# Optimization experiments

Measured on AMD Instinct MI355X. Metric: run time of the kernel, lower is better.

The kernel has to match this reference:

```python
import jax, jax.numpy as jnp
import numpy as np

B, L, M, F = 64, 1024, 256, 256


def setup_inputs() -> dict:
    key = jax.random.key(0)
    k1, k2 = jax.random.split(key)
    patch_features = jax.random.normal(k1, (B, L, F), dtype=jnp.float32)
    queue = jax.random.normal(k2, (L, M, F), dtype=jnp.float32)
    return {"patch_features": patch_features, "queue": queue}


def reference(patch_features, queue):
    # sim[b, l, m] = <patch_features[b, l], queue[l, m]>  (batched per-location matmul)
    sim = jnp.einsum('blf,lmf->blm', patch_features, queue)
    # original takes topk(5) then keeps only index 0 == argmax over memory slots
    idx = jnp.argmax(sim, axis=-1)                      # [B, L]
    # N[b, l] = queue[l, idx[b, l]]
    N = queue[jnp.arange(queue.shape[0])[None, :], idx]  # [B, L, F]
    return N
```

## Files before the change

kernel.cpp:

```cpp
#include <hip/hip_runtime.h>

#define B_ 64
#define L_ 1024
#define M_ 256
#define F_ 256

typedef __attribute__((ext_vector_type(8))) short short8;
typedef __attribute__((ext_vector_type(16))) float f32x16;
typedef unsigned int u32;

struct Frag3 { short8 h, m, l; };

__device__ __forceinline__ u32 asu(float f) { union { float f; u32 u; } c; c.f = f; return c.u; }
__device__ __forceinline__ float asf(u32 u) { union { float f; u32 u; } c; c.u = u; return c.f; }
__device__ __forceinline__ u32 pack2(u32 lo, u32 hi) {
    return __builtin_amdgcn_perm(hi, lo, 0x07060302u);
}
__device__ __forceinline__ float4 ld4(const float* p) {
    return *reinterpret_cast<const float4*>(p);
}

__device__ __forceinline__ void async_cp16(const float* g, float* l) {
    __builtin_amdgcn_global_load_lds(
        (const __attribute__((address_space(1))) u32*)g,
        (__attribute__((address_space(3))) u32*)l,
        16, 0, 0);
}

__device__ __forceinline__ Frag3 split8(float4 a, float4 b) {
    float x[8] = {a.x, a.y, a.z, a.w, b.x, b.y, b.z, b.w};
    u32 xb[8], rb[8], sb[8];
#pragma unroll
    for (int e = 0; e < 8; ++e) {
        xb[e] = asu(x[e]);
        float hf = asf(xb[e] & 0xFFFF0000u);
        float r  = x[e] - hf;
        rb[e] = asu(r);
        float mf = asf(rb[e] & 0xFFFF0000u);
        float r2 = r - mf;
        sb[e] = asu(r2);
    }
    union { u32 w[4]; short8 s; } H, M, Lo;
#pragma unroll
    for (int d = 0; d < 4; ++d) {
        H.w[d]  = pack2(xb[2 * d], xb[2 * d + 1]);
        M.w[d]  = pack2(rb[2 * d], rb[2 * d + 1]);
        Lo.w[d] = pack2(sb[2 * d], sb[2 * d + 1]);
    }
    Frag3 f; f.h = H.s; f.m = M.s; f.l = Lo.s; return f;
}

#define MFMA6(ACC, A, Bf)                                                        \
    ACC = __builtin_amdgcn_mfma_f32_32x32x16_bf16((A).m, (Bf).m, ACC, 0, 0, 0);  \
    ACC = __builtin_amdgcn_mfma_f32_32x32x16_bf16((A).h, (Bf).l, ACC, 0, 0, 0);  \
    ACC = __builtin_amdgcn_mfma_f32_32x32x16_bf16((A).l, (Bf).h, ACC, 0, 0, 0);  \
    ACC = __builtin_amdgcn_mfma_f32_32x32x16_bf16((A).h, (Bf).m, ACC, 0, 0, 0);  \
    ACC = __builtin_amdgcn_mfma_f32_32x32x16_bf16((A).m, (Bf).h, ACC, 0, 0, 0);  \
    ACC = __builtin_amdgcn_mfma_f32_32x32x16_bf16((A).h, (Bf).h, ACC, 0, 0, 0)

__launch_bounds__(256, 2)
__global__ void mq_mfma_lds_kernel(const float* __restrict__ patch,
                                   const float* __restrict__ queue,
                                   float* __restrict__ out) {
    const int l    = blockIdx.x;
    const int t    = threadIdx.x;
    const int lane = t & 63;
    const int w    = t >> 6;
    const int bt   = w & 1;
    const int mtg  = w >> 1;
    const int r32  = lane & 31;
    const int kh   = lane >> 5;

    __shared__ __align__(16) float Ql[2][256 * 32];
    __shared__ __align__(16) float Pl[2][64 * 32];

    const int lrow = lane >> 3;
    const int lcol = lane & 7;
    const float* qsrcw = queue + ((size_t)l * M_ + w * 64 + lrow) * F_ + (lcol ^ lrow) * 4;
    const float* psrcw = patch + ((size_t)(w * 16 + lrow) * L_ + l) * F_ + (lcol ^ lrow) * 4;

#define STAGE(FT, BUF)                                                            \
    {                                                                             \
        _Pragma("unroll")                                                         \
        for (int k = 0; k < 8; ++k)                                               \
            async_cp16(qsrcw + (size_t)k * 8 * F_ + (FT) * 32,                    \
                       &Ql[BUF][(w * 8 + k) * 256]);                              \
        _Pragma("unroll")                                                         \
        for (int k = 0; k < 2; ++k)                                               \
            async_cp16(psrcw + (size_t)k * 8 * L_ * F_ + (FT) * 32,               \
                       &Pl[BUF][(w * 2 + k) * 256]);                              \
    }

    f32x16 acc[4];
#pragma unroll
    for (int mt = 0; mt < 4; ++mt) acc[mt] = (f32x16)0.f;

    STAGE(0, 0);

    const int s7 = r32 & 7;
    const int ra = bt * 32 + r32;

#pragma unroll 1
    for (int ft = 0; ft < 8; ++ft) {
        __builtin_amdgcn_s_barrier();
        __builtin_amdgcn_sched_barrier(0);
        if (ft < 7) {
            STAGE(ft + 1, (ft + 1) & 1);
            asm volatile("s_waitcnt vmcnt(10)" ::: "memory");
        } else {
            asm volatile("s_waitcnt vmcnt(0)" ::: "memory");
        }
        __builtin_amdgcn_sched_barrier(0);
        __builtin_amdgcn_s_barrier();
        __builtin_amdgcn_sched_barrier(0);

        const float* Qb = Ql[ft & 1];
        const float* Pb = Pl[ft & 1];
#pragma unroll
        for (int kk = 0; kk < 2; ++kk) {
            const int c0 = kk * 4 + kh * 2;
            const float4 a0 = ld4(&Pb[ra * 32 + ((c0 ^ s7) * 4)]);
            const float4 a1 = ld4(&Pb[ra * 32 + (((c0 + 1) ^ s7) * 4)]);
            const Frag3 A = split8(a0, a1);
#pragma unroll
            for (int mt = 0; mt < 4; ++mt) {
                const int rb = mtg * 128 + mt * 32 + r32;
                const float4 b0 = ld4(&Qb[rb * 32 + ((c0 ^ s7) * 4)]);
                const float4 b1 = ld4(&Qb[rb * 32 + (((c0 + 1) ^ s7) * 4)]);
                const Frag3 Bf = split8(b0, b1);
                MFMA6(acc[mt], A, Bf);
            }
        }
    }

    __syncthreads();

    float* pval = (float*)&Pl[0][0];
    int*   pidx = (int*)&Pl[0][0] + 128;
    int*   sidx = (int*)&Pl[0][0] + 256;
#pragma unroll
    for (int r = 0; r < 16; ++r) {
        float bv = acc[0][r];
        int   bi = mtg * 128 + r32;
#pragma unroll
        for (int mt = 1; mt < 4; ++mt) {
            const float cv = acc[mt][r];
            const int   ci = mtg * 128 + mt * 32 + r32;
            if (cv > bv) { bv = cv; bi = ci; }
        }
#pragma unroll
        for (int off = 16; off >= 1; off >>= 1) {
            const float ov = __shfl_xor(bv, off);
            const int   oi = __shfl_xor(bi, off);
            if (ov > bv || (ov == bv && oi < bi)) { bv = ov; bi = oi; }
        }
        if (r32 == 0) {
            const int b = bt * 32 + (r & 3) + 8 * (r >> 2) + 4 * kh;
            pval[mtg * 64 + b] = bv;
            pidx[mtg * 64 + b] = bi;
        }
    }
    __syncthreads();

    if (t < 64) {
        const float v0 = pval[t], v1 = pval[64 + t];
        sidx[t] = (v1 > v0) ? pidx[64 + t] : pidx[t];
    }
    __syncthreads();

    const int cb = t >> 6;
    const int cc = t & 63;
#pragma unroll
    for (int b0 = 0; b0 < 64; b0 += 4) {
        const int b  = b0 + cb;
        const int mi = sidx[b];
        const float4 v = ld4(&queue[((size_t)l * M_ + mi) * F_ + cc * 4]);
        *reinterpret_cast<float4*>(&out[((size_t)b * L_ + l) * F_ + cc * 4]) = v;
    }
}

extern "C" void kernel_launch(void* const* d_in, const int* in_sizes, int n_in,
                              void* d_out, int out_size, void* d_ws, size_t ws_size,
                              hipStream_t stream) {
    const float* patch = (const float*)d_in[0];
    const float* queue = (const float*)d_in[1];
    float* out = (float*)d_out;
    mq_mfma_lds_kernel<<<dim3(L_), dim3(256), 0, stream>>>(patch, queue, out);
}
```

Before: 105.9 us.

## Use 512 threads per block, splitting memory slots across eight waves

```diff
diff --git a/kernel.cpp b/kernel.cpp
--- a/kernel.cpp
+++ b/kernel.cpp
@@ -58,7 +58,7 @@
     ACC = __builtin_amdgcn_mfma_f32_32x32x16_bf16((A).m, (Bf).h, ACC, 0, 0, 0);  \
     ACC = __builtin_amdgcn_mfma_f32_32x32x16_bf16((A).h, (Bf).h, ACC, 0, 0, 0)
 
-__launch_bounds__(256, 2)
+__launch_bounds__(512, 2)
 __global__ void mq_mfma_lds_kernel(const float* __restrict__ patch,
                                    const float* __restrict__ queue,
                                    float* __restrict__ out) {
@@ -76,29 +76,26 @@
 
     const int lrow = lane >> 3;
     const int lcol = lane & 7;
-    const float* qsrcw = queue + ((size_t)l * M_ + w * 64 + lrow) * F_ + (lcol ^ lrow) * 4;
-    const float* psrcw = patch + ((size_t)(w * 16 + lrow) * L_ + l) * F_ + (lcol ^ lrow) * 4;
+    const float* qsrcw = queue + ((size_t)l * M_ + w * 32 + lrow) * F_ + (lcol ^ lrow) * 4;
+    const float* psrcw = patch + ((size_t)(w * 8 + lrow) * L_ + l) * F_ + (lcol ^ lrow) * 4;
 
 #define STAGE(FT, BUF)                                                            \
     {                                                                             \
         _Pragma("unroll")                                                         \
-        for (int k = 0; k < 8; ++k)                                               \
+        for (int k = 0; k < 4; ++k)                                               \
             async_cp16(qsrcw + (size_t)k * 8 * F_ + (FT) * 32,                    \
-                       &Ql[BUF][(w * 8 + k) * 256]);                              \
-        _Pragma("unroll")                                                         \
-        for (int k = 0; k < 2; ++k)                                               \
-            async_cp16(psrcw + (size_t)k * 8 * L_ * F_ + (FT) * 32,               \
-                       &Pl[BUF][(w * 2 + k) * 256]);                              \
+                       &Ql[BUF][(w * 4 + k) * 256]);                              \
+        async_cp16(psrcw + (FT) * 32, &Pl[BUF][w * 256]);                         \
     }
 
-    f32x16 acc[4];
-#pragma unroll
-    for (int mt = 0; mt < 4; ++mt) acc[mt] = (f32x16)0.f;
+    f32x16 acc0 = (f32x16)0.f, acc1 = (f32x16)0.f;
 
     STAGE(0, 0);
 
     const int s7 = r32 & 7;
     const int ra = bt * 32 + r32;
+    const int rb0 = mtg * 64 + r32;
+    const int rb1 = mtg * 64 + 32 + r32;
 
 #pragma unroll 1
     for (int ft = 0; ft < 8; ++ft) {
@@ -106,7 +103,7 @@
         __builtin_amdgcn_sched_barrier(0);
         if (ft < 7) {
             STAGE(ft + 1, (ft + 1) & 1);
-            asm volatile("s_waitcnt vmcnt(10)" ::: "memory");
+            asm volatile("s_waitcnt vmcnt(5)" ::: "memory");
         } else {
             asm volatile("s_waitcnt vmcnt(0)" ::: "memory");
         }
@@ -122,13 +119,17 @@
             const float4 a0 = ld4(&Pb[ra * 32 + ((c0 ^ s7) * 4)]);
             const float4 a1 = ld4(&Pb[ra * 32 + (((c0 + 1) ^ s7) * 4)]);
             const Frag3 A = split8(a0, a1);
-#pragma unroll
-            for (int mt = 0; mt < 4; ++mt) {
-                const int rb = mtg * 128 + mt * 32 + r32;
-                const float4 b0 = ld4(&Qb[rb * 32 + ((c0 ^ s7) * 4)]);
-                const float4 b1 = ld4(&Qb[rb * 32 + (((c0 + 1) ^ s7) * 4)]);
+            {
+                const float4 b0 = ld4(&Qb[rb0 * 32 + ((c0 ^ s7) * 4)]);
+                const float4 b1 = ld4(&Qb[rb0 * 32 + (((c0 + 1) ^ s7) * 4)]);
                 const Frag3 Bf = split8(b0, b1);
-                MFMA6(acc[mt], A, Bf);
+                MFMA6(acc0, A, Bf);
+            }
+            {
+                const float4 b0 = ld4(&Qb[rb1 * 32 + ((c0 ^ s7) * 4)]);
+                const float4 b1 = ld4(&Qb[rb1 * 32 + (((c0 + 1) ^ s7) * 4)]);
+                const Frag3 Bf = split8(b0, b1);
+                MFMA6(acc1, A, Bf);
             }
         }
     }
@@ -136,16 +137,15 @@
     __syncthreads();
 
     float* pval = (float*)&Pl[0][0];
-    int*   pidx = (int*)&Pl[0][0] + 128;
-    int*   sidx = (int*)&Pl[0][0] + 256;
+    int*   pidx = (int*)&Pl[0][0] + 256;
+    int*   sidx = (int*)&Pl[0][0] + 512;
 #pragma unroll
     for (int r = 0; r < 16; ++r) {
-        float bv = acc[0][r];
-        int   bi = mtg * 128 + r32;
-#pragma unroll
-        for (int mt = 1; mt < 4; ++mt) {
-            const float cv = acc[mt][r];
-            const int   ci = mtg * 128 + mt * 32 + r32;
+        float bv = acc0[r];
+        int   bi = mtg * 64 + r32;
+        {
+            const float cv = acc1[r];
+            const int   ci = mtg * 64 + 32 + r32;
             if (cv > bv) { bv = cv; bi = ci; }
         }
 #pragma unroll
@@ -163,15 +163,21 @@
     __syncthreads();
 
     if (t < 64) {
-        const float v0 = pval[t], v1 = pval[64 + t];
-        sidx[t] = (v1 > v0) ? pidx[64 + t] : pidx[t];
+        float bv = pval[t];
+        int   bi = pidx[t];
+#pragma unroll
+        for (int g = 1; g < 4; ++g) {
+            const float cv = pval[g * 64 + t];
+            if (cv > bv) { bv = cv; bi = pidx[g * 64 + t]; }
+        }
+        sidx[t] = bi;
     }
     __syncthreads();
 
     const int cb = t >> 6;
     const int cc = t & 63;
 #pragma unroll
-    for (int b0 = 0; b0 < 64; b0 += 4) {
+    for (int b0 = 0; b0 < 64; b0 += 8) {
         const int b  = b0 + cb;
         const int mi = sidx[b];
         const float4 v = ld4(&queue[((size_t)l * M_ + mi) * F_ + cc * 4]);
@@ -185,5 +191,5 @@
     const float* patch = (const float*)d_in[0];
     const float* queue = (const float*)d_in[1];
     float* out = (float*)d_out;
-    mq_mfma_lds_kernel<<<dim3(L_), dim3(256), 0, stream>>>(patch, queue, out);
+    mq_mfma_lds_kernel<<<dim3(L_), dim3(512), 0, stream>>>(patch, queue, out);
 }
```

New measurement: 103.5 us. 2.3% less time.

## Drop LDS double buffering to single buffer for higher block occupancy

Applied to the files above, without the earlier changes.

```diff
diff --git a/kernel.cpp b/kernel.cpp
--- a/kernel.cpp
+++ b/kernel.cpp
@@ -59,7 +59,7 @@
     ACC = __builtin_amdgcn_mfma_f32_32x32x16_bf16((A).h, (Bf).h, ACC, 0, 0, 0)
 
 __launch_bounds__(256, 2)
-__global__ void mq_mfma_lds_kernel(const float* __restrict__ patch,
+__global__ void mq_mfma_sb4_kernel(const float* __restrict__ patch,
                                    const float* __restrict__ queue,
                                    float* __restrict__ out) {
     const int l    = blockIdx.x;
@@ -71,31 +71,17 @@
     const int r32  = lane & 31;
     const int kh   = lane >> 5;
 
-    __shared__ __align__(16) float Ql[2][256 * 32];
-    __shared__ __align__(16) float Pl[2][64 * 32];
+    __shared__ __align__(16) float Ql[256 * 32];
+    __shared__ __align__(16) float Pl[64 * 32];
 
     const int lrow = lane >> 3;
     const int lcol = lane & 7;
     const float* qsrcw = queue + ((size_t)l * M_ + w * 64 + lrow) * F_ + (lcol ^ lrow) * 4;
     const float* psrcw = patch + ((size_t)(w * 16 + lrow) * L_ + l) * F_ + (lcol ^ lrow) * 4;
 
-#define STAGE(FT, BUF)                                                            \
-    {                                                                             \
-        _Pragma("unroll")                                                         \
-        for (int k = 0; k < 8; ++k)                                               \
-            async_cp16(qsrcw + (size_t)k * 8 * F_ + (FT) * 32,                    \
-                       &Ql[BUF][(w * 8 + k) * 256]);                              \
-        _Pragma("unroll")                                                         \
-        for (int k = 0; k < 2; ++k)                                               \
-            async_cp16(psrcw + (size_t)k * 8 * L_ * F_ + (FT) * 32,               \
-                       &Pl[BUF][(w * 2 + k) * 256]);                              \
-    }
-
     f32x16 acc[4];
 #pragma unroll
     for (int mt = 0; mt < 4; ++mt) acc[mt] = (f32x16)0.f;
-
-    STAGE(0, 0);
 
     const int s7 = r32 & 7;
     const int ra = bt * 32 + r32;
@@ -104,29 +90,31 @@
     for (int ft = 0; ft < 8; ++ft) {
         __builtin_amdgcn_s_barrier();
         __builtin_amdgcn_sched_barrier(0);
-        if (ft < 7) {
-            STAGE(ft + 1, (ft + 1) & 1);
-            asm volatile("s_waitcnt vmcnt(10)" ::: "memory");
-        } else {
-            asm volatile("s_waitcnt vmcnt(0)" ::: "memory");
+        {
+            const int o = ft * 32;
+#pragma unroll
+            for (int k = 0; k < 8; ++k)
+                async_cp16(qsrcw + (size_t)k * 8 * F_ + o, &Ql[(w * 8 + k) * 256]);
+#pragma unroll
+            for (int k = 0; k < 2; ++k)
+                async_cp16(psrcw + (size_t)k * 8 * L_ * F_ + o, &Pl[(w * 2 + k) * 256]);
         }
+        asm volatile("s_waitcnt vmcnt(0)" ::: "memory");
         __builtin_amdgcn_sched_barrier(0);
         __builtin_amdgcn_s_barrier();
         __builtin_amdgcn_sched_barrier(0);
 
-        const float* Qb = Ql[ft & 1];
-        const float* Pb = Pl[ft & 1];
 #pragma unroll
         for (int kk = 0; kk < 2; ++kk) {
             const int c0 = kk * 4 + kh * 2;
-            const float4 a0 = ld4(&Pb[ra * 32 + ((c0 ^ s7) * 4)]);
-            const float4 a1 = ld4(&Pb[ra * 32 + (((c0 + 1) ^ s7) * 4)]);
+            const float4 a0 = ld4(&Pl[ra * 32 + ((c0 ^ s7) * 4)]);
+            const float4 a1 = ld4(&Pl[ra * 32 + (((c0 + 1) ^ s7) * 4)]);
             const Frag3 A = split8(a0, a1);
 #pragma unroll
             for (int mt = 0; mt < 4; ++mt) {
                 const int rb = mtg * 128 + mt * 32 + r32;
-                const float4 b0 = ld4(&Qb[rb * 32 + ((c0 ^ s7) * 4)]);
-                const float4 b1 = ld4(&Qb[rb * 32 + (((c0 + 1) ^ s7) * 4)]);
+                const float4 b0 = ld4(&Ql[rb * 32 + ((c0 ^ s7) * 4)]);
+                const float4 b1 = ld4(&Ql[rb * 32 + (((c0 + 1) ^ s7) * 4)]);
                 const Frag3 Bf = split8(b0, b1);
                 MFMA6(acc[mt], A, Bf);
             }
@@ -135,9 +123,9 @@
 
     __syncthreads();
 
-    float* pval = (float*)&Pl[0][0];
-    int*   pidx = (int*)&Pl[0][0] + 128;
-    int*   sidx = (int*)&Pl[0][0] + 256;
+    float* pval = (float*)&Pl[0];
+    int*   pidx = (int*)&Pl[0] + 128;
+    int*   sidx = (int*)&Pl[0] + 256;
 #pragma unroll
     for (int r = 0; r < 16; ++r) {
         float bv = acc[0][r];
@@ -185,5 +173,5 @@
     const float* patch = (const float*)d_in[0];
     const float* queue = (const float*)d_in[1];
     float* out = (float*)d_out;
-    mq_mfma_lds_kernel<<<dim3(L_), dim3(256), 0, stream>>>(patch, queue, out);
+    mq_mfma_sb4_kernel<<<dim3(L_), dim3(256), 0, stream>>>(patch, queue, out);
 }
```

New measurement: 106.7 us. Within noise of the previous version (+0.7%).
